# Optimization experiments

Hardware: AMD Instinct MI355X
Metric: run time of the kernel (lower is better)

Reference implementation:

```python
import jax, jax.numpy as jnp
import numpy as np

D_MODEL = 1024
N_HEADS = 16
HEAD_DIM = D_MODEL // N_HEADS
FF_DIM = 4096
EPS = 1e-5


def _layer_norm(v, g, b):
    mu = jnp.mean(v, axis=-1, keepdims=True)
    var = jnp.mean(jnp.square(v - mu), axis=-1, keepdims=True)
    return (v - mu) * jax.lax.rsqrt(var + EPS) * g + b


def setup_inputs() -> dict:
    key = jax.random.key(0)
    ks = jax.random.split(key, 16)
    s = 0.02
    x = jax.random.normal(ks[0], (2, 2048, D_MODEL), dtype=jnp.float32)
    Wq = jax.random.normal(ks[1], (D_MODEL, D_MODEL), dtype=jnp.float32) * s
    Wk = jax.random.normal(ks[2], (D_MODEL, D_MODEL), dtype=jnp.float32) * s
    Wv = jax.random.normal(ks[3], (D_MODEL, D_MODEL), dtype=jnp.float32) * s
    Wo = jax.random.normal(ks[4], (D_MODEL, D_MODEL), dtype=jnp.float32) * s
    bq = jnp.zeros((D_MODEL,), jnp.float32)
    bk = jnp.zeros((D_MODEL,), jnp.float32)
    bv = jnp.zeros((D_MODEL,), jnp.float32)
    bo = jnp.zeros((D_MODEL,), jnp.float32)
    # per-head Conv1d(kernel=1) == per-head linear; weights [H, out, in]
    W1 = jax.random.normal(ks[5], (N_HEADS, FF_DIM, HEAD_DIM), dtype=jnp.float32) * s
    b1 = jnp.zeros((N_HEADS, FF_DIM), jnp.float32)
    W2 = jax.random.normal(ks[6], (N_HEADS, HEAD_DIM, FF_DIM), dtype=jnp.float32) * s
    b2 = jnp.zeros((N_HEADS, HEAD_DIM), jnp.float32)
    g1 = jnp.ones((D_MODEL,), jnp.float32)
    be1 = jnp.zeros((D_MODEL,), jnp.float32)
    g2 = jnp.ones((D_MODEL,), jnp.float32)
    be2 = jnp.zeros((D_MODEL,), jnp.float32)
    return {"x": x, "Wq": Wq, "bq": bq, "Wk": Wk, "bk": bk, "Wv": Wv, "bv": bv,
            "Wo": Wo, "bo": bo, "W1": W1, "b1": b1, "W2": W2, "b2": b2,
            "g1": g1, "be1": be1, "g2": g2, "be2": be2}


def reference(x, Wq, bq, Wk, bk, Wv, bv, Wo, bo, W1, b1, W2, b2, g1, be1, g2, be2):
    B, S, D = x.shape
    H, hd = N_HEADS, HEAD_DIM
    # --- multi-head self-attention (standard scaled dot-product) ---
    q = (x @ Wq + bq).reshape(B, S, H, hd)
    k = (x @ Wk + bk).reshape(B, S, H, hd)
    v = (x @ Wv + bv).reshape(B, S, H, hd)
    scores = jnp.einsum('bqhd,bkhd->bhqk', q, k) / jnp.sqrt(jnp.float32(hd))
    attn = jax.nn.softmax(scores, axis=-1)          # [B,H,S,S]
    ctx = jnp.einsum('bhqk,bkhd->bqhd', attn, v).reshape(B, S, D)
    residual = ctx @ Wo + bo
    # dropout is identity in eval mode
    x1 = _layer_norm(x + residual, g1, be1)
    # --- per-head feed-forward (Conv1d kernel=1 per head, batched over heads) ---
    xh = x1.reshape(B, S, H, hd)
    h = jax.nn.relu(jnp.einsum('bshd,hfd->bshf', xh, W1) + b1)   # [B,S,H,FF]
    ff = jnp.einsum('bshf,hdf->bshd', h, W2) + b2                 # [B,S,H,hd]
    y = _layer_norm(x1 + ff.reshape(B, S, D), g2, be2)
    return (y, attn)
```

## Files before the change

kernel.cpp:

```cpp
#include <hip/hip_runtime.h>
#include <cstddef>

#define D_M 1024
#define NH 16
#define HD 64
#define FFD 4096
#define SQ 2048
#define BB 2
#define TOK (BB*SQ)
#define EPS 1e-5f

typedef __attribute__((ext_vector_type(8))) short bf16x8;
typedef __attribute__((ext_vector_type(4))) float f32x4;

__device__ inline unsigned short f32_bf16_rne(float f) {
  unsigned int u = __float_as_uint(f);
  unsigned int r = (u + 0x7fffu + ((u >> 16) & 1u)) >> 16;
  return (unsigned short)r;
}

__device__ inline float wave_sum(float v) {
  #pragma unroll
  for (int m = 32; m >= 1; m >>= 1) v += __shfl_xor(v, m);
  return v;
}

__global__ __launch_bounds__(256)
void convert_bf16_k(const float* __restrict__ src, unsigned short* __restrict__ dst, int n4) {
  int i = blockIdx.x * 256 + threadIdx.x;
  if (i >= n4) return;
  float4 v = ((const float4*)src)[i];
  ushort4 h;
  h.x = f32_bf16_rne(v.x); h.y = f32_bf16_rne(v.y);
  h.z = f32_bf16_rne(v.z); h.w = f32_bf16_rne(v.w);
  ((ushort4*)dst)[i] = h;
}

__global__ __launch_bounds__(256)
void transp4_k(const float* __restrict__ W0, const float* __restrict__ W1_,
               const float* __restrict__ W2_, const float* __restrict__ W3,
               unsigned short* __restrict__ h0, unsigned short* __restrict__ h1,
               unsigned short* __restrict__ h2, unsigned short* __restrict__ h3) {
  const float* W; unsigned short* hT;
  switch (blockIdx.z) {
    case 0: W = W0; hT = h0; break;
    case 1: W = W1_; hT = h1; break;
    case 2: W = W2_; hT = h2; break;
    default: W = W3; hT = h3; break;
  }
  __shared__ float tile[64][65];
  const int bn = blockIdx.x * 64;
  const int bk = blockIdx.y * 64;
  const int t = threadIdx.x;
  #pragma unroll
  for (int i = 0; i < 4; ++i) {
    int r = (t >> 4) + i * 16, c = (t & 15) * 4;
    float4 v = *(const float4*)&W[(size_t)(bk + r) * D_M + bn + c];
    tile[r][c] = v.x; tile[r][c + 1] = v.y; tile[r][c + 2] = v.z; tile[r][c + 3] = v.w;
  }
  __syncthreads();
  #pragma unroll
  for (int i = 0; i < 4; ++i) {
    int n = (t >> 4) + i * 16, k = (t & 15) * 4;
    ushort4 h;
    h.x = f32_bf16_rne(tile[k][n]);     h.y = f32_bf16_rne(tile[k + 1][n]);
    h.z = f32_bf16_rne(tile[k + 2][n]); h.w = f32_bf16_rne(tile[k + 3][n]);
    *(ushort4*)&hT[(size_t)(bn + n) * D_M + bk + k] = h;
  }
}

__global__ __launch_bounds__(256)
void qkv_gemm_k(const unsigned short* __restrict__ xh_g,
                const unsigned short* __restrict__ Bqh, const unsigned short* __restrict__ Bkh,
                const unsigned short* __restrict__ Bvh,
                const float* __restrict__ bq, const float* __restrict__ bk, const float* __restrict__ bv,
                unsigned short* __restrict__ qh, unsigned short* __restrict__ kh,
                unsigned short* __restrict__ vth) {
  constexpr int LDK = 40;
  __shared__ unsigned short Ah[64 * LDK];
  __shared__ unsigned short Bh[3][128 * LDK];
  const int tid = threadIdx.x;
  const int wave = tid >> 6, lane = tid & 63;
  const int wm = (wave >> 1) * 32, wn = (wave & 1) * 64;
  const int bn = blockIdx.x * 128, bm = blockIdx.y * 64;
  const int K = D_M;

  f32x4 acc[3][2][4] = {};
  const int sr = tid >> 2, sk = (tid & 3) * 8;
  const int l15 = lane & 15, k8 = (lane >> 4) * 8;

  const unsigned short* Bhp[3] = {Bqh, Bkh, Bvh};

  for (int k0 = 0; k0 < K; k0 += 32) {
    *(uint4*)&Ah[sr * LDK + sk] = *(const uint4*)&xh_g[(size_t)(bm + sr) * K + k0 + sk];
    #pragma unroll
    for (int s = 0; s < 3; ++s) {
      #pragma unroll
      for (int c = 0; c < 2; ++c) {
        int r = sr + c * 64;
        *(uint4*)&Bh[s][r * LDK + sk] = *(const uint4*)&Bhp[s][(size_t)(bn + r) * K + k0 + sk];
      }
    }
    __syncthreads();
    bf16x8 af[2];
    #pragma unroll
    for (int m = 0; m < 2; ++m)
      af[m] = *(bf16x8*)&Ah[(wm + m * 16 + l15) * LDK + k8];
    #pragma unroll
    for (int s = 0; s < 3; ++s) {
      #pragma unroll
      for (int n = 0; n < 4; ++n) {
        bf16x8 b0 = *(bf16x8*)&Bh[s][(wn + n * 16 + l15) * LDK + k8];
        #pragma unroll
        for (int m = 0; m < 2; ++m) {
          if (s == 2) {
            acc[s][m][n] = __builtin_amdgcn_mfma_f32_16x16x32_bf16(af[m], b0, acc[s][m][n], 0, 0, 0);
          } else {
            acc[s][m][n] = __builtin_amdgcn_mfma_f32_16x16x32_bf16(b0, af[m], acc[s][m][n], 0, 0, 0);
          }
        }
      }
    }
    __syncthreads();
  }
  const int kq4 = (lane >> 4) * 4;
  #pragma unroll
  for (int s = 0; s < 2; ++s) {
    const float* bias = (s == 0) ? bq : bk;
    unsigned short* oh = (s == 0) ? qh : kh;
    #pragma unroll
    for (int n = 0; n < 4; ++n) {
      int colb = bn + wn + n * 16 + kq4;
      float4 bv4 = *(const float4*)&bias[colb];
      #pragma unroll
      for (int m = 0; m < 2; ++m) {
        int tok = bm + wm + m * 16 + l15;
        ushort4 h;
        h.x = f32_bf16_rne(acc[s][m][n][0] + bv4.x);
        h.y = f32_bf16_rne(acc[s][m][n][1] + bv4.y);
        h.z = f32_bf16_rne(acc[s][m][n][2] + bv4.z);
        h.w = f32_bf16_rne(acc[s][m][n][3] + bv4.w);
        *(ushort4*)&oh[(size_t)tok * D_M + colb] = h;
      }
    }
  }
  #pragma unroll
  for (int n = 0; n < 4; ++n) {
    int col = bn + wn + n * 16 + l15;
    float bvv = bv[col];
    #pragma unroll
    for (int m = 0; m < 2; ++m) {
      int row0 = bm + wm + m * 16 + kq4;
      ushort4 hv;
      hv.x = f32_bf16_rne(acc[2][m][n][0] + bvv); hv.y = f32_bf16_rne(acc[2][m][n][1] + bvv);
      hv.z = f32_bf16_rne(acc[2][m][n][2] + bvv); hv.w = f32_bf16_rne(acc[2][m][n][3] + bvv);
      size_t idx = (((size_t)(row0 >> 11) * NH + (col >> 6)) * HD + (col & 63)) * SQ + (row0 & 2047);
      *(ushort4*)&vth[idx] = hv;
    }
  }
}

__global__ __launch_bounds__(256)
void proj_gemm_k(const unsigned short* __restrict__ Ah_g,
                 const unsigned short* __restrict__ Bh_g,
                 const float* __restrict__ bias, float* __restrict__ C,
                 int M, int N, int K) {
  constexpr int LDK = 40;
  __shared__ unsigned short Ah[64 * LDK];
  __shared__ unsigned short Bh[128 * LDK];
  const int tid = threadIdx.x;
  const int wave = tid >> 6, lane = tid & 63;
  const int wm = (wave >> 1) * 32, wn = (wave & 1) * 64;
  const int bn = blockIdx.x * 128, bm = blockIdx.y * 64;

  f32x4 acc[2][4] = {};
  const int sr = tid >> 2, sk = (tid & 3) * 8;
  const int l15 = lane & 15, k8 = (lane >> 4) * 8;

  for (int k0 = 0; k0 < K; k0 += 32) {
    *(uint4*)&Ah[sr * LDK + sk] = *(const uint4*)&Ah_g[(size_t)(bm + sr) * K + k0 + sk];
    #pragma unroll
    for (int c = 0; c < 2; ++c) {
      int r = sr + c * 64;
      *(uint4*)&Bh[r * LDK + sk] = *(const uint4*)&Bh_g[(size_t)(bn + r) * K + k0 + sk];
    }
    __syncthreads();
    bf16x8 af[2], bfr[4];
    #pragma unroll
    for (int m = 0; m < 2; ++m)
      af[m] = *(bf16x8*)&Ah[(wm + m * 16 + l15) * LDK + k8];
    #pragma unroll
    for (int n = 0; n < 4; ++n)
      bfr[n] = *(bf16x8*)&Bh[(wn + n * 16 + l15) * LDK + k8];
    #pragma unroll
    for (int m = 0; m < 2; ++m)
      #pragma unroll
      for (int n = 0; n < 4; ++n)
        acc[m][n] = __builtin_amdgcn_mfma_f32_16x16x32_bf16(bfr[n], af[m], acc[m][n], 0, 0, 0);
    __syncthreads();
  }
  const int kq4 = (lane >> 4) * 4;
  #pragma unroll
  for (int n = 0; n < 4; ++n) {
    int colb = bn + wn + n * 16 + kq4;
    float4 bv4 = *(const float4*)&bias[colb];
    #pragma unroll
    for (int m = 0; m < 2; ++m) {
      int tok = bm + wm + m * 16 + l15;
      float4 v = {acc[m][n][0] + bv4.x, acc[m][n][1] + bv4.y,
                  acc[m][n][2] + bv4.z, acc[m][n][3] + bv4.w};
      *(float4*)&C[(size_t)tok * N + colb] = v;
    }
  }
}

__global__ __launch_bounds__(256)
void fused_attn_k(const unsigned short* __restrict__ qh,
                  const unsigned short* __restrict__ kh,
                  const unsigned short* __restrict__ vth,
                  float* __restrict__ attn,
                  unsigned short* __restrict__ ctxh) {
  constexpr int LDK = 72;
  constexpr int NT = SQ / 64;
  __shared__ unsigned short Kth[2][64 * LDK], Vts[2][64 * LDK];
  __shared__ unsigned short Ph[128 * LDK];
  const int tid = threadIdx.x, wave = tid >> 6, lane = tid & 63;
  const int l15 = lane & 15, kq = lane >> 4;
  const int bh = blockIdx.x, b = bh >> 4, h = bh & 15;
  const int q0 = blockIdx.y * 128;

  bf16x8 qfh[2][2];
  #pragma unroll
  for (int qi = 0; qi < 2; ++qi) {
    const size_t qoff = (size_t)(b * SQ + q0 + wave * 32 + qi * 16 + l15) * D_M + h * HD + kq * 8;
    qfh[qi][0] = *(const bf16x8*)&qh[qoff];  qfh[qi][1] = *(const bf16x8*)&qh[qoff + 32];
  }

  const size_t kbase = (size_t)(b * SQ) * D_M + h * HD;
  const size_t vbase = (size_t)bh * HD * SQ;
  const int srow = tid >> 2, sc = (tid & 3) * 16;

  float lsum[2] = {0.f, 0.f};
  {
    const unsigned short* src = &kh[kbase + (size_t)srow * D_M + sc];
    *(uint4*)&Kth[0][srow * LDK + sc] = *(const uint4*)src;
    *(uint4*)&Kth[0][srow * LDK + sc + 8] = *(const uint4*)(src + 8);
  }
  __syncthreads();
  for (int t = 0; t < NT; ++t) {
    const int cur = t & 1;
    const bool pf = (t + 1 < NT);
    uint4 r0, r1;
    if (pf) {
      const unsigned short* src = &kh[kbase + (size_t)((t + 1) * 64 + srow) * D_M + sc];
      r0 = *(const uint4*)src;
      r1 = *(const uint4*)(src + 8);
    }
    #pragma unroll
    for (int n = 0; n < 4; ++n) {
      bf16x8 kb0 = *(bf16x8*)&Kth[cur][(n * 16 + l15) * LDK + kq * 8];
      bf16x8 kb1 = *(bf16x8*)&Kth[cur][(n * 16 + l15) * LDK + 32 + kq * 8];
      #pragma unroll
      for (int qi = 0; qi < 2; ++qi) {
        f32x4 s = {};
        s = __builtin_amdgcn_mfma_f32_16x16x32_bf16(kb0, qfh[qi][0], s, 0, 0, 0);
        s = __builtin_amdgcn_mfma_f32_16x16x32_bf16(kb1, qfh[qi][1], s, 0, 0, 0);
        #pragma unroll
        for (int r = 0; r < 4; ++r) lsum[qi] += __expf(s[r] * 0.125f);
      }
    }
    if (pf) {
      *(uint4*)&Kth[cur ^ 1][srow * LDK + sc] = r0;
      *(uint4*)&Kth[cur ^ 1][srow * LDK + sc + 8] = r1;
    }
    __syncthreads();
  }
  float invl[2];
  #pragma unroll
  for (int qi = 0; qi < 2; ++qi) {
    float l = lsum[qi];
    l += __shfl_xor(l, 16);
    l += __shfl_xor(l, 32);
    invl[qi] = 1.0f / l;
  }

  f32x4 cacc[2][4] = {};
  {
    const unsigned short* srch = &kh[kbase + (size_t)srow * D_M + sc];
    const unsigned short* srcv = &vth[vbase + (size_t)srow * SQ + sc];
    *(uint4*)&Kth[0][srow * LDK + sc] = *(const uint4*)srch;
    *(uint4*)&Kth[0][srow * LDK + sc + 8] = *(const uint4*)(srch + 8);
    *(uint4*)&Vts[0][srow * LDK + sc] = *(const uint4*)srcv;
    *(uint4*)&Vts[0][srow * LDK + sc + 8] = *(const uint4*)(srcv + 8);
  }
  __syncthreads();
  for (int t = 0; t < NT; ++t) {
    const int cur = t & 1;
    const int k0 = t * 64;
    const bool pf = (t + 1 < NT);
    uint4 rk0, rk1, rv0, rv1;
    if (pf) {
      const unsigned short* srch = &kh[kbase + (size_t)(k0 + 64 + srow) * D_M + sc];
      const unsigned short* srcv = &vth[vbase + (size_t)srow * SQ + k0 + 64 + sc];
      rk0 = *(const uint4*)srch; rk1 = *(const uint4*)(srch + 8);
      rv0 = *(const uint4*)srcv; rv1 = *(const uint4*)(srcv + 8);
    }
    #pragma unroll
    for (int n = 0; n < 4; ++n) {
      bf16x8 kb0 = *(bf16x8*)&Kth[cur][(n * 16 + l15) * LDK + kq * 8];
      bf16x8 kb1 = *(bf16x8*)&Kth[cur][(n * 16 + l15) * LDK + 32 + kq * 8];
      #pragma unroll
      for (int qi = 0; qi < 2; ++qi) {
        f32x4 s = {};
        s = __builtin_amdgcn_mfma_f32_16x16x32_bf16(kb0, qfh[qi][0], s, 0, 0, 0);
        s = __builtin_amdgcn_mfma_f32_16x16x32_bf16(kb1, qfh[qi][1], s, 0, 0, 0);
        float4 pv;
        pv.x = __expf(s[0] * 0.125f) * invl[qi];
        pv.y = __expf(s[1] * 0.125f) * invl[qi];
        pv.z = __expf(s[2] * 0.125f) * invl[qi];
        pv.w = __expf(s[3] * 0.125f) * invl[qi];
        const int qrow = wave * 32 + qi * 16 + l15;
        *(float4*)&attn[((size_t)bh * SQ + q0 + qrow) * SQ + k0 + n * 16 + kq * 4] = pv;
        ushort4 p4;
        p4.x = f32_bf16_rne(pv.x); p4.y = f32_bf16_rne(pv.y);
        p4.z = f32_bf16_rne(pv.z); p4.w = f32_bf16_rne(pv.w);
        *(ushort4*)&Ph[qrow * LDK + n * 16 + kq * 4] = p4;
      }
    }
    #pragma unroll
    for (int qi = 0; qi < 2; ++qi) {
      bf16x8 pa0 = *(bf16x8*)&Ph[(wave * 32 + qi * 16 + l15) * LDK + kq * 8];
      bf16x8 pa1 = *(bf16x8*)&Ph[(wave * 32 + qi * 16 + l15) * LDK + 32 + kq * 8];
      #pragma unroll
      for (int n = 0; n < 4; ++n) {
        bf16x8 vb0 = *(bf16x8*)&Vts[cur][(n * 16 + l15) * LDK + kq * 8];
        bf16x8 vb1 = *(bf16x8*)&Vts[cur][(n * 16 + l15) * LDK + 32 + kq * 8];
        cacc[qi][n] = __builtin_amdgcn_mfma_f32_16x16x32_bf16(vb0, pa0, cacc[qi][n], 0, 0, 0);
        cacc[qi][n] = __builtin_amdgcn_mfma_f32_16x16x32_bf16(vb1, pa1, cacc[qi][n], 0, 0, 0);
      }
    }
    if (pf) {
      *(uint4*)&Kth[cur ^ 1][srow * LDK + sc] = rk0;
      *(uint4*)&Kth[cur ^ 1][srow * LDK + sc + 8] = rk1;
      *(uint4*)&Vts[cur ^ 1][srow * LDK + sc] = rv0;
      *(uint4*)&Vts[cur ^ 1][srow * LDK + sc + 8] = rv1;
    }
    __syncthreads();
  }
  #pragma unroll
  for (int qi = 0; qi < 2; ++qi)
    #pragma unroll
    for (int n = 0; n < 4; ++n) {
      ushort4 hh;
      hh.x = f32_bf16_rne(cacc[qi][n][0]); hh.y = f32_bf16_rne(cacc[qi][n][1]);
      hh.z = f32_bf16_rne(cacc[qi][n][2]); hh.w = f32_bf16_rne(cacc[qi][n][3]);
      size_t off = (size_t)(b * SQ + q0 + wave * 32 + qi * 16 + l15) * D_M + h * HD + n * 16 + kq * 4;
      *(ushort4*)&ctxh[off] = hh;
    }
}

__global__ __launch_bounds__(256)
void ff_bf16_k(const unsigned short* __restrict__ x1h,
               const unsigned short* __restrict__ W1h_, const float* __restrict__ b1,
               const unsigned short* __restrict__ W2h_, const float* __restrict__ b2,
               float* __restrict__ out) {
  constexpr int LDW = 72;
  constexpr int LDH = 40;
  __shared__ unsigned short W1sh[2][32 * LDW];
  __shared__ unsigned short W2sh[2][64 * LDH];
  __shared__ unsigned short Hh[128 * LDH];

  const int tid = threadIdx.x;
  const int wave = tid >> 6, lane = tid & 63;
  const int wm = wave >> 1, wf = wave & 1, wd = wave & 1;
  const int h = blockIdx.x;
  const int m0 = blockIdx.y * 128;
  const int l15 = lane & 15, kq = lane >> 4;

  const size_t w1base = (size_t)h * FFD * HD;
  const size_t w2base = (size_t)h * HD * FFD;
  const int r1 = tid >> 3, k1 = (tid & 7) * 8;
  const int r2 = tid >> 2, f2 = (tid & 3) * 8;

  bf16x8 xf[4][2];
  #pragma unroll
  for (int m = 0; m < 4; ++m)
    #pragma unroll
    for (int ks = 0; ks < 2; ++ks) {
      size_t gof = (size_t)(m0 + wm * 64 + m * 16 + l15) * D_M + h * HD + ks * 32 + kq * 8;
      xf[m][ks] = *(const bf16x8*)&x1h[gof];
    }

  {
    *(uint4*)&W1sh[0][r1 * LDW + k1] = *(const uint4*)&W1h_[w1base + (size_t)r1 * HD + k1];
    *(uint4*)&W2sh[0][r2 * LDH + f2] = *(const uint4*)&W2h_[w2base + (size_t)r2 * FFD + f2];
  }
  __syncthreads();

  f32x4 ffacc[4][2] = {};

  for (int ch = 0; ch < FFD / 32; ++ch) {
    const int buf = ch & 1;
    const bool pf = (ch + 1 < FFD / 32);
    uint4 w1h_r, w2h_r;
    if (pf) {
      const int f0n = (ch + 1) * 32;
      w1h_r = *(const uint4*)&W1h_[w1base + (size_t)(f0n + r1) * HD + k1];
      w2h_r = *(const uint4*)&W2h_[w2base + (size_t)r2 * FFD + f0n + f2];
    }
    f32x4 hacc[4] = {};
    #pragma unroll
    for (int ks = 0; ks < 2; ++ks) {
      bf16x8 w1h = *(bf16x8*)&W1sh[buf][(wf * 16 + l15) * LDW + ks * 32 + kq * 8];
      #pragma unroll
      for (int m = 0; m < 4; ++m)
        hacc[m] = __builtin_amdgcn_mfma_f32_16x16x32_bf16(w1h, xf[m][ks], hacc[m], 0, 0, 0);
    }
    {
      const int fb = wf * 16 + kq * 4;
      float4 b1v = *(const float4*)&b1[(size_t)h * FFD + ch * 32 + fb];
      const float bb[4] = {b1v.x, b1v.y, b1v.z, b1v.w};
      #pragma unroll
      for (int m = 0; m < 4; ++m) {
        int tok = wm * 64 + m * 16 + l15;
        ushort4 hh;
        hh.x = f32_bf16_rne(fmaxf(hacc[m][0] + bb[0], 0.0f));
        hh.y = f32_bf16_rne(fmaxf(hacc[m][1] + bb[1], 0.0f));
        hh.z = f32_bf16_rne(fmaxf(hacc[m][2] + bb[2], 0.0f));
        hh.w = f32_bf16_rne(fmaxf(hacc[m][3] + bb[3], 0.0f));
        *(ushort4*)&Hh[tok * LDH + fb] = hh;
      }
    }
    __syncthreads();
    bf16x8 hfr[4];
    #pragma unroll
    for (int m = 0; m < 4; ++m)
      hfr[m] = *(bf16x8*)&Hh[(wm * 64 + m * 16 + l15) * LDH + kq * 8];
    #pragma unroll
    for (int n = 0; n < 2; ++n) {
      bf16x8 w2h = *(bf16x8*)&W2sh[buf][(wd * 32 + n * 16 + l15) * LDH + kq * 8];
      #pragma unroll
      for (int m = 0; m < 4; ++m)
        ffacc[m][n] = __builtin_amdgcn_mfma_f32_16x16x32_bf16(w2h, hfr[m], ffacc[m][n], 0, 0, 0);
    }
    if (pf) {
      *(uint4*)&W1sh[buf ^ 1][r1 * LDW + k1] = w1h_r;
      *(uint4*)&W2sh[buf ^ 1][r2 * LDH + f2] = w2h_r;
    }
    __syncthreads();
  }
  #pragma unroll
  for (int n = 0; n < 2; ++n) {
    int db = wd * 32 + n * 16 + kq * 4;
    float4 b2v = *(const float4*)&b2[(size_t)h * HD + db];
    #pragma unroll
    for (int m = 0; m < 4; ++m) {
      int tok = m0 + wm * 64 + m * 16 + l15;
      float4 v = {ffacc[m][n][0] + b2v.x, ffacc[m][n][1] + b2v.y,
                  ffacc[m][n][2] + b2v.z, ffacc[m][n][3] + b2v.w};
      *(float4*)&out[(size_t)tok * D_M + h * HD + db] = v;
    }
  }
}

template<int BF16OUT>
__global__ __launch_bounds__(256)
void add_ln_kernel(const float* __restrict__ a, const float* __restrict__ r,
                   const float* __restrict__ g, const float* __restrict__ be,
                   float* __restrict__ out, unsigned short* __restrict__ oh) {
  const size_t row = blockIdx.x;
  const int tid = threadIdx.x;
  __shared__ float red1[4];
  __shared__ float red2[4];
  float4 va = ((const float4*)(a + row * D_M))[tid];
  float4 vr = ((const float4*)(r + row * D_M))[tid];
  float v0 = va.x + vr.x, v1 = va.y + vr.y, v2 = va.z + vr.z, v3 = va.w + vr.w;
  float s = v0 + v1 + v2 + v3;
  float sq = v0 * v0 + v1 * v1 + v2 * v2 + v3 * v3;
  s = wave_sum(s);
  sq = wave_sum(sq);
  if ((tid & 63) == 0) { red1[tid >> 6] = s; red2[tid >> 6] = sq; }
  __syncthreads();
  s = red1[0] + red1[1] + red1[2] + red1[3];
  sq = red2[0] + red2[1] + red2[2] + red2[3];
  const float mu = s * (1.0f / D_M);
  const float var = sq * (1.0f / D_M) - mu * mu;
  float x = var + EPS;
  float rs = rsqrtf(x);
  rs = rs * (1.5f - 0.5f * x * rs * rs);
  float4 gg = ((const float4*)g)[tid];
  float4 bb = ((const float4*)be)[tid];
  float4 o = {(v0 - mu) * rs * gg.x + bb.x, (v1 - mu) * rs * gg.y + bb.y,
              (v2 - mu) * rs * gg.z + bb.z, (v3 - mu) * rs * gg.w + bb.w};
  ((float4*)(out + row * D_M))[tid] = o;
  if (BF16OUT) {
    ushort4 h;
    h.x = f32_bf16_rne(o.x); h.y = f32_bf16_rne(o.y);
    h.z = f32_bf16_rne(o.z); h.w = f32_bf16_rne(o.w);
    ((ushort4*)(oh + row * D_M))[tid] = h;
  }
}

extern "C" void kernel_launch(void* const* d_in, const int* in_sizes, int n_in,
                              void* d_out, int out_size, void* d_ws, size_t ws_size,
                              hipStream_t stream) {
  const float* x   = (const float*)d_in[0];
  const float* Wq  = (const float*)d_in[1];
  const float* bq  = (const float*)d_in[2];
  const float* Wk  = (const float*)d_in[3];
  const float* bk  = (const float*)d_in[4];
  const float* Wv  = (const float*)d_in[5];
  const float* bv  = (const float*)d_in[6];
  const float* Wo  = (const float*)d_in[7];
  const float* bo  = (const float*)d_in[8];
  const float* W1  = (const float*)d_in[9];
  const float* b1  = (const float*)d_in[10];
  const float* W2  = (const float*)d_in[11];
  const float* b2  = (const float*)d_in[12];
  const float* g1  = (const float*)d_in[13];
  const float* be1 = (const float*)d_in[14];
  const float* g2  = (const float*)d_in[15];
  const float* be2 = (const float*)d_in[16];

  float* y_out = (float*)d_out;
  float* attn  = (float*)d_out + (size_t)TOK * D_M;

  char* p = (char*)d_ws;
  const size_t MB = 1024 * 1024;
  unsigned short* WqT = (unsigned short*)(p + 0 * MB);
  unsigned short* WkT = (unsigned short*)(p + 2 * MB);
  unsigned short* WvT = (unsigned short*)(p + 4 * MB);
  unsigned short* WoT = (unsigned short*)(p + 6 * MB);
  unsigned short* xh  = (unsigned short*)(p + 8 * MB);
  unsigned short* qh  = (unsigned short*)(p + 16 * MB);
  unsigned short* kh  = (unsigned short*)(p + 24 * MB);
  unsigned short* vth = (unsigned short*)(p + 32 * MB);
  unsigned short* ctxh = (unsigned short*)(p + 40 * MB);
  float* resid = (float*)(p + 48 * MB);
  float* x1b   = (float*)(p + 64 * MB);
  unsigned short* x1c_h = (unsigned short*)(p + 8 * MB);
  unsigned short* W1c_h = (unsigned short*)(p + 16 * MB);
  unsigned short* W2c_h = (unsigned short*)(p + 24 * MB);
  float* ffb = (float*)(p + 32 * MB);

  const dim3 blk(256);
  const int n4_act = TOK * D_M / 4;

  transp4_k<<<dim3(16, 16, 4), blk, 0, stream>>>(Wq, Wk, Wv, Wo, WqT, WkT, WvT, WoT);
  convert_bf16_k<<<dim3(n4_act / 256), blk, 0, stream>>>(x, xh, n4_act);

  qkv_gemm_k<<<dim3(D_M / 128, TOK / 64), blk, 0, stream>>>(
      xh, WqT, WkT, WvT, bq, bk, bv, qh, kh, vth);

  fused_attn_k<<<dim3(BB * NH, SQ / 128), blk, 0, stream>>>(qh, kh, vth, attn, ctxh);

  proj_gemm_k<<<dim3(D_M / 128, TOK / 64), blk, 0, stream>>>(
      ctxh, WoT, bo, resid, TOK, D_M, D_M);
  add_ln_kernel<1><<<dim3(TOK), blk, 0, stream>>>(x, resid, g1, be1, x1b, x1c_h);

  convert_bf16_k<<<dim3(n4_act / 256), blk, 0, stream>>>(W1, W1c_h, n4_act);
  convert_bf16_k<<<dim3(n4_act / 256), blk, 0, stream>>>(W2, W2c_h, n4_act);
  ff_bf16_k<<<dim3(NH, TOK / 128), blk, 0, stream>>>(x1c_h, W1c_h, b1, W2c_h, b2, ffb);
  add_ln_kernel<0><<<dim3(TOK), blk, 0, stream>>>(x1b, ffb, g2, be2, y_out, nullptr);
}
```

Measured before the change: 477.1 us.

## Widen attention stats pass tiles, remap FF waves, merge weight conversions

The attention kernel's row-sum pass now loads 128 keys per iteration into a shared arena, which halves the number of barriers and loop trips. The shared buffers are merged into one arena that is reused by both passes. The per-head feed-forward kernel changes its wave mapping so each wave owns 32 tokens and all 32 FF features, and it drops one __syncthreads per chunk because each wave only reads the Hh rows it wrote itself. The two W1/W2 bf16 conversion launches are merged into one 2D launch to cut launch overhead.

```diff
diff --git a/kernel.cpp b/kernel.cpp
--- a/kernel.cpp
+++ b/kernel.cpp
@@ -23,6 +23,20 @@
   #pragma unroll
   for (int m = 32; m >= 1; m >>= 1) v += __shfl_xor(v, m);
   return v;
+}
+
+__global__ __launch_bounds__(256)
+void convert2_bf16_k(const float* __restrict__ s0, unsigned short* __restrict__ d0,
+                     const float* __restrict__ s1, unsigned short* __restrict__ d1, int n4) {
+  const float* src = blockIdx.y ? s1 : s0;
+  unsigned short* dst = blockIdx.y ? d1 : d0;
+  int i = blockIdx.x * 256 + threadIdx.x;
+  if (i >= n4) return;
+  float4 v = ((const float4*)src)[i];
+  ushort4 h;
+  h.x = f32_bf16_rne(v.x); h.y = f32_bf16_rne(v.y);
+  h.z = f32_bf16_rne(v.z); h.w = f32_bf16_rne(v.w);
+  ((ushort4*)dst)[i] = h;
 }
 
 __global__ __launch_bounds__(256)
@@ -221,9 +235,7 @@
                   float* __restrict__ attn,
                   unsigned short* __restrict__ ctxh) {
   constexpr int LDK = 72;
-  constexpr int NT = SQ / 64;
-  __shared__ unsigned short Kth[2][64 * LDK], Vts[2][64 * LDK];
-  __shared__ unsigned short Ph[128 * LDK];
+  __shared__ unsigned short arena[6 * 64 * LDK];
   const int tid = threadIdx.x, wave = tid >> 6, lane = tid & 63;
   const int l15 = lane & 15, kq = lane >> 4;
   const int bh = blockIdx.x, b = bh >> 4, h = bh & 15;
@@ -242,24 +254,31 @@
 
   float lsum[2] = {0.f, 0.f};
   {
-    const unsigned short* src = &kh[kbase + (size_t)srow * D_M + sc];
-    *(uint4*)&Kth[0][srow * LDK + sc] = *(const uint4*)src;
-    *(uint4*)&Kth[0][srow * LDK + sc + 8] = *(const uint4*)(src + 8);
+    #pragma unroll
+    for (int hlf = 0; hlf < 2; ++hlf) {
+      const int row = srow + hlf * 64;
+      const unsigned short* src = &kh[kbase + (size_t)row * D_M + sc];
+      *(uint4*)&arena[row * LDK + sc] = *(const uint4*)src;
+      *(uint4*)&arena[row * LDK + sc + 8] = *(const uint4*)(src + 8);
+    }
   }
   __syncthreads();
-  for (int t = 0; t < NT; ++t) {
-    const int cur = t & 1;
-    const bool pf = (t + 1 < NT);
-    uint4 r0, r1;
+  for (int t = 0; t < SQ / 128; ++t) {
+    const int abuf = (t & 1) * 9216;
+    const bool pf = (t + 1 < SQ / 128);
+    uint4 r0[2], r1[2];
     if (pf) {
-      const unsigned short* src = &kh[kbase + (size_t)((t + 1) * 64 + srow) * D_M + sc];
-      r0 = *(const uint4*)src;
-      r1 = *(const uint4*)(src + 8);
-    }
-    #pragma unroll
-    for (int n = 0; n < 4; ++n) {
-      bf16x8 kb0 = *(bf16x8*)&Kth[cur][(n * 16 + l15) * LDK + kq * 8];
-      bf16x8 kb1 = *(bf16x8*)&Kth[cur][(n * 16 + l15) * LDK + 32 + kq * 8];
+      #pragma unroll
+      for (int hlf = 0; hlf < 2; ++hlf) {
+        const unsigned short* src = &kh[kbase + (size_t)((t + 1) * 128 + srow + hlf * 64) * D_M + sc];
+        r0[hlf] = *(const uint4*)src;
+        r1[hlf] = *(const uint4*)(src + 8);
+      }
+    }
+    #pragma unroll
+    for (int n = 0; n < 8; ++n) {
+      bf16x8 kb0 = *(bf16x8*)&arena[abuf + (n * 16 + l15) * LDK + kq * 8];
+      bf16x8 kb1 = *(bf16x8*)&arena[abuf + (n * 16 + l15) * LDK + 32 + kq * 8];
       #pragma unroll
       for (int qi = 0; qi < 2; ++qi) {
         f32x4 s = {};
@@ -270,8 +289,13 @@
       }
     }
     if (pf) {
-      *(uint4*)&Kth[cur ^ 1][srow * LDK + sc] = r0;
-      *(uint4*)&Kth[cur ^ 1][srow * LDK + sc + 8] = r1;
+      const int nbuf = ((t + 1) & 1) * 9216;
+      #pragma unroll
+      for (int hlf = 0; hlf < 2; ++hlf) {
+        const int row = srow + hlf * 64;
+        *(uint4*)&arena[nbuf + row * LDK + sc] = r0[hlf];
+        *(uint4*)&arena[nbuf + row * LDK + sc + 8] = r1[hlf];
+      }
     }
     __syncthreads();
   }
@@ -284,20 +308,22 @@
     invl[qi] = 1.0f / l;
   }
 
+  unsigned short* Ph = arena + 18432;
   f32x4 cacc[2][4] = {};
   {
     const unsigned short* srch = &kh[kbase + (size_t)srow * D_M + sc];
     const unsigned short* srcv = &vth[vbase + (size_t)srow * SQ + sc];
-    *(uint4*)&Kth[0][srow * LDK + sc] = *(const uint4*)srch;
-    *(uint4*)&Kth[0][srow * LDK + sc + 8] = *(const uint4*)(srch + 8);
-    *(uint4*)&Vts[0][srow * LDK + sc] = *(const uint4*)srcv;
-    *(uint4*)&Vts[0][srow * LDK + sc + 8] = *(const uint4*)(srcv + 8);
+    *(uint4*)&arena[srow * LDK + sc] = *(const uint4*)srch;
+    *(uint4*)&arena[srow * LDK + sc + 8] = *(const uint4*)(srch + 8);
+    *(uint4*)&arena[9216 + srow * LDK + sc] = *(const uint4*)srcv;
+    *(uint4*)&arena[9216 + srow * LDK + sc + 8] = *(const uint4*)(srcv + 8);
   }
   __syncthreads();
-  for (int t = 0; t < NT; ++t) {
-    const int cur = t & 1;
+  for (int t = 0; t < SQ / 64; ++t) {
+    const int kbuf = (t & 1) * 4608;
+    const int vbuf = 9216 + (t & 1) * 4608;
     const int k0 = t * 64;
-    const bool pf = (t + 1 < NT);
+    const bool pf = (t + 1 < SQ / 64);
     uint4 rk0, rk1, rv0, rv1;
     if (pf) {
       const unsigned short* srch = &kh[kbase + (size_t)(k0 + 64 + srow) * D_M + sc];
@@ -307,8 +333,8 @@
     }
     #pragma unroll
     for (int n = 0; n < 4; ++n) {
-      bf16x8 kb0 = *(bf16x8*)&Kth[cur][(n * 16 + l15) * LDK + kq * 8];
-      bf16x8 kb1 = *(bf16x8*)&Kth[cur][(n * 16 + l15) * LDK + 32 + kq * 8];
+      bf16x8 kb0 = *(bf16x8*)&arena[kbuf + (n * 16 + l15) * LDK + kq * 8];
+      bf16x8 kb1 = *(bf16x8*)&arena[kbuf + (n * 16 + l15) * LDK + 32 + kq * 8];
       #pragma unroll
       for (int qi = 0; qi < 2; ++qi) {
         f32x4 s = {};
@@ -333,17 +359,19 @@
       bf16x8 pa1 = *(bf16x8*)&Ph[(wave * 32 + qi * 16 + l15) * LDK + 32 + kq * 8];
       #pragma unroll
       for (int n = 0; n < 4; ++n) {
-        bf16x8 vb0 = *(bf16x8*)&Vts[cur][(n * 16 + l15) * LDK + kq * 8];
-        bf16x8 vb1 = *(bf16x8*)&Vts[cur][(n * 16 + l15) * LDK + 32 + kq * 8];
+        bf16x8 vb0 = *(bf16x8*)&arena[vbuf + (n * 16 + l15) * LDK + kq * 8];
+        bf16x8 vb1 = *(bf16x8*)&arena[vbuf + (n * 16 + l15) * LDK + 32 + kq * 8];
         cacc[qi][n] = __builtin_amdgcn_mfma_f32_16x16x32_bf16(vb0, pa0, cacc[qi][n], 0, 0, 0);
         cacc[qi][n] = __builtin_amdgcn_mfma_f32_16x16x32_bf16(vb1, pa1, cacc[qi][n], 0, 0, 0);
       }
     }
     if (pf) {
-      *(uint4*)&Kth[cur ^ 1][srow * LDK + sc] = rk0;
-      *(uint4*)&Kth[cur ^ 1][srow * LDK + sc + 8] = rk1;
-      *(uint4*)&Vts[cur ^ 1][srow * LDK + sc] = rv0;
-      *(uint4*)&Vts[cur ^ 1][srow * LDK + sc + 8] = rv1;
+      const int nk = ((t + 1) & 1) * 4608;
+      const int nv = 9216 + ((t + 1) & 1) * 4608;
+      *(uint4*)&arena[nk + srow * LDK + sc] = rk0;
+      *(uint4*)&arena[nk + srow * LDK + sc + 8] = rk1;
+      *(uint4*)&arena[nv + srow * LDK + sc] = rv0;
+      *(uint4*)&arena[nv + srow * LDK + sc + 8] = rv1;
     }
     __syncthreads();
   }
@@ -372,7 +400,6 @@
 
   const int tid = threadIdx.x;
   const int wave = tid >> 6, lane = tid & 63;
-  const int wm = wave >> 1, wf = wave & 1, wd = wave & 1;
   const int h = blockIdx.x;
   const int m0 = blockIdx.y * 128;
   const int l15 = lane & 15, kq = lane >> 4;
@@ -382,12 +409,12 @@
   const int r1 = tid >> 3, k1 = (tid & 7) * 8;
   const int r2 = tid >> 2, f2 = (tid & 3) * 8;
 
-  bf16x8 xf[4][2];
-  #pragma unroll
-  for (int m = 0; m < 4; ++m)
+  bf16x8 xf[2][2];
+  #pragma unroll
+  for (int m = 0; m < 2; ++m)
     #pragma unroll
     for (int ks = 0; ks < 2; ++ks) {
-      size_t gof = (size_t)(m0 + wm * 64 + m * 16 + l15) * D_M + h * HD + ks * 32 + kq * 8;
+      size_t gof = (size_t)(m0 + wave * 32 + m * 16 + l15) * D_M + h * HD + ks * 32 + kq * 8;
       xf[m][ks] = *(const bf16x8*)&x1h[gof];
     }
 
@@ -397,7 +424,7 @@
   }
   __syncthreads();
 
-  f32x4 ffacc[4][2] = {};
+  f32x4 ffacc[2][4] = {};
 
   for (int ch = 0; ch < FFD / 32; ++ch) {
     const int buf = ch & 1;
@@ -408,40 +435,42 @@
       w1h_r = *(const uint4*)&W1h_[w1base + (size_t)(f0n + r1) * HD + k1];
       w2h_r = *(const uint4*)&W2h_[w2base + (size_t)r2 * FFD + f0n + f2];
     }
-    f32x4 hacc[4] = {};
+    f32x4 hacc[2][2] = {};
     #pragma unroll
     for (int ks = 0; ks < 2; ++ks) {
-      bf16x8 w1h = *(bf16x8*)&W1sh[buf][(wf * 16 + l15) * LDW + ks * 32 + kq * 8];
-      #pragma unroll
-      for (int m = 0; m < 4; ++m)
-        hacc[m] = __builtin_amdgcn_mfma_f32_16x16x32_bf16(w1h, xf[m][ks], hacc[m], 0, 0, 0);
-    }
-    {
-      const int fb = wf * 16 + kq * 4;
+      #pragma unroll
+      for (int nf = 0; nf < 2; ++nf) {
+        bf16x8 w1f = *(bf16x8*)&W1sh[buf][(nf * 16 + l15) * LDW + ks * 32 + kq * 8];
+        #pragma unroll
+        for (int m = 0; m < 2; ++m)
+          hacc[nf][m] = __builtin_amdgcn_mfma_f32_16x16x32_bf16(w1f, xf[m][ks], hacc[nf][m], 0, 0, 0);
+      }
+    }
+    #pragma unroll
+    for (int nf = 0; nf < 2; ++nf) {
+      const int fb = nf * 16 + kq * 4;
       float4 b1v = *(const float4*)&b1[(size_t)h * FFD + ch * 32 + fb];
-      const float bb[4] = {b1v.x, b1v.y, b1v.z, b1v.w};
-      #pragma unroll
-      for (int m = 0; m < 4; ++m) {
-        int tok = wm * 64 + m * 16 + l15;
+      #pragma unroll
+      for (int m = 0; m < 2; ++m) {
+        int tok = wave * 32 + m * 16 + l15;
         ushort4 hh;
-        hh.x = f32_bf16_rne(fmaxf(hacc[m][0] + bb[0], 0.0f));
-        hh.y = f32_bf16_rne(fmaxf(hacc[m][1] + bb[1], 0.0f));
-        hh.z = f32_bf16_rne(fmaxf(hacc[m][2] + bb[2], 0.0f));
-        hh.w = f32_bf16_rne(fmaxf(hacc[m][3] + bb[3], 0.0f));
+        hh.x = f32_bf16_rne(fmaxf(hacc[nf][m][0] + b1v.x, 0.0f));
+        hh.y = f32_bf16_rne(fmaxf(hacc[nf][m][1] + b1v.y, 0.0f));
+        hh.z = f32_bf16_rne(fmaxf(hacc[nf][m][2] + b1v.z, 0.0f));
+        hh.w = f32_bf16_rne(fmaxf(hacc[nf][m][3] + b1v.w, 0.0f));
         *(ushort4*)&Hh[tok * LDH + fb] = hh;
       }
     }
-    __syncthreads();
-    bf16x8 hfr[4];
-    #pragma unroll
-    for (int m = 0; m < 4; ++m)
-      hfr[m] = *(bf16x8*)&Hh[(wm * 64 + m * 16 + l15) * LDH + kq * 8];
-    #pragma unroll
-    for (int n = 0; n < 2; ++n) {
-      bf16x8 w2h = *(bf16x8*)&W2sh[buf][(wd * 32 + n * 16 + l15) * LDH + kq * 8];
-      #pragma unroll
-      for (int m = 0; m < 4; ++m)
-        ffacc[m][n] = __builtin_amdgcn_mfma_f32_16x16x32_bf16(w2h, hfr[m], ffacc[m][n], 0, 0, 0);
+    bf16x8 hfr[2];
+    #pragma unroll
+    for (int m = 0; m < 2; ++m)
+      hfr[m] = *(bf16x8*)&Hh[(wave * 32 + m * 16 + l15) * LDH + kq * 8];
+    #pragma unroll
+    for (int n = 0; n < 4; ++n) {
+      bf16x8 w2f = *(bf16x8*)&W2sh[buf][(n * 16 + l15) * LDH + kq * 8];
+      #pragma unroll
+      for (int m = 0; m < 2; ++m)
+        ffacc[m][n] = __builtin_amdgcn_mfma_f32_16x16x32_bf16(w2f, hfr[m], ffacc[m][n], 0, 0, 0);
     }
     if (pf) {
       *(uint4*)&W1sh[buf ^ 1][r1 * LDW + k1] = w1h_r;
@@ -450,12 +479,12 @@
     __syncthreads();
   }
   #pragma unroll
-  for (int n = 0; n < 2; ++n) {
-    int db = wd * 32 + n * 16 + kq * 4;
+  for (int n = 0; n < 4; ++n) {
+    int db = n * 16 + kq * 4;
     float4 b2v = *(const float4*)&b2[(size_t)h * HD + db];
     #pragma unroll
-    for (int m = 0; m < 4; ++m) {
-      int tok = m0 + wm * 64 + m * 16 + l15;
+    for (int m = 0; m < 2; ++m) {
+      int tok = m0 + wave * 32 + m * 16 + l15;
       float4 v = {ffacc[m][n][0] + b2v.x, ffacc[m][n][1] + b2v.y,
                   ffacc[m][n][2] + b2v.z, ffacc[m][n][3] + b2v.w};
       *(float4*)&out[(size_t)tok * D_M + h * HD + db] = v;
@@ -558,8 +587,7 @@
       ctxh, WoT, bo, resid, TOK, D_M, D_M);
   add_ln_kernel<1><<<dim3(TOK), blk, 0, stream>>>(x, resid, g1, be1, x1b, x1c_h);
 
-  convert_bf16_k<<<dim3(n4_act / 256), blk, 0, stream>>>(W1, W1c_h, n4_act);
-  convert_bf16_k<<<dim3(n4_act / 256), blk, 0, stream>>>(W2, W2c_h, n4_act);
+  convert2_bf16_k<<<dim3(n4_act / 256, 2), blk, 0, stream>>>(W1, W1c_h, W2, W2c_h, n4_act);
   ff_bf16_k<<<dim3(NH, TOK / 128), blk, 0, stream>>>(x1c_h, W1c_h, b1, W2c_h, b2, ffb);
   add_ln_kernel<0><<<dim3(TOK), blk, 0, stream>>>(x1b, ffb, g2, be2, y_out, nullptr);
 }
```

New measurement: 513.3 us. +7.6%, slower.
